# Performance work log

Hardware: AMD Instinct MI355X
Metric: run time of the kernel (lower is better)

Reference implementation:

```python
import jax, jax.numpy as jnp
import numpy as np

B, T, D_Q, D_K, D_W = 128, 4096, 16, 16, 32


def setup_inputs() -> dict:
    key0 = jax.random.key(0)
    ks = jax.random.split(key0, 8)
    return {
        "query": jax.random.normal(ks[0], (B, 1, D_Q), dtype=jnp.float32),
        "key": jax.random.normal(ks[1], (B, T, D_K), dtype=jnp.float32),
        "value": jax.random.normal(ks[2], (B, T, D_K), dtype=jnp.float32),
        "W1": jax.random.normal(ks[3], (D_W, D_Q), dtype=jnp.float32) * 0.1,
        "W2": jax.random.normal(ks[4], (D_W, D_K), dtype=jnp.float32) * 0.1,
        "bias": jax.random.uniform(ks[5], (), dtype=jnp.float32, minval=-0.1, maxval=0.1),
        "v_w": jax.random.normal(ks[6], (1, D_W), dtype=jnp.float32) * 0.1,
        "v_b": jax.random.normal(ks[7], (1,), dtype=jnp.float32) * 0.1,
    }


def reference(query, key, value, W1, W2, bias, v_w, v_b):
    # Bahdanau additive attention.
    # query: [B,1,d_q], key/value: [B,T,d_k]
    q_proj = jnp.einsum('bqd,wd->bqw', query, W1)      # [B,1,d_w]
    k_proj = jnp.einsum('btd,wd->btw', key, W2)        # [B,T,d_w]
    h = jnp.tanh(k_proj + q_proj + bias)               # [B,T,d_w]
    score = (jnp.einsum('btw,ow->bto', h, v_w) + v_b).squeeze(-1)  # [B,T]
    attn = jax.nn.softmax(score, axis=-1)              # [B,T]
    context = jnp.einsum('bt,btd->bd', attn, value)[:, None, :]    # [B,1,d_v]
    return context, attn
```

## Files before the change

### kernel.cpp

```cpp
#include <hip/hip_runtime.h>

#define NB 128
#define NT 4096
#define DKD 16
#define DW 32
#define CHUNKS 16
#define TC 256
#define BLK 256
#define BLK2 128

__device__ __forceinline__ float fast_tanh(float x) {
    float e = __expf(2.0f * x);
    return 1.0f - 2.0f * __builtin_amdgcn_rcpf(e + 1.0f);
}

__global__ __launch_bounds__(BLK, 6) void aa_score(
    const float* __restrict__ query, const float* __restrict__ key,
    const float* __restrict__ value, const float* __restrict__ W1,
    const float* __restrict__ W2, const float* __restrict__ bias,
    const float* __restrict__ v_w, const float* __restrict__ v_b,
    float* __restrict__ attn,
    float* __restrict__ ws_l,
    float* __restrict__ ws_ctx)
{
    const int b   = blockIdx.x >> 4;
    const int c   = blockIdx.x & 15;
    const int tid = threadIdx.x;

    __shared__ float s_comb[DW];
    __shared__ float s_rctx[4 * 16];
    __shared__ float s_rl[4];

    const size_t tbase = (size_t)b * NT + (size_t)c * TC + tid;
    const float4* kp = reinterpret_cast<const float4*>(key)   + tbase * 4;
    const float4* vp = reinterpret_cast<const float4*>(value) + tbase * 4;
    const float4 k0 = kp[0], k1 = kp[1], k2 = kp[2], k3 = kp[3];

    if (tid < DW) {
        const int w = tid;
        float acc = bias[0];
        const float* q  = query + b * DKD;
        const float* w1 = W1 + w * DKD;
        #pragma unroll
        for (int d = 0; d < DKD; ++d) acc = fmaf(q[d], w1[d], acc);
        s_comb[w] = acc;
    }
    __syncthreads();

    const float vb = v_b[0];
    float sc = vb;

    #pragma unroll
    for (int w = 0; w < DW; ++w) {
        const float* wr = W2 + w * DKD;
        float h = s_comb[w];
        h = fmaf(k0.x, wr[ 0], h); h = fmaf(k0.y, wr[ 1], h);
        h = fmaf(k0.z, wr[ 2], h); h = fmaf(k0.w, wr[ 3], h);
        h = fmaf(k1.x, wr[ 4], h); h = fmaf(k1.y, wr[ 5], h);
        h = fmaf(k1.z, wr[ 6], h); h = fmaf(k1.w, wr[ 7], h);
        h = fmaf(k2.x, wr[ 8], h); h = fmaf(k2.y, wr[ 9], h);
        h = fmaf(k2.z, wr[10], h); h = fmaf(k2.w, wr[11], h);
        h = fmaf(k3.x, wr[12], h); h = fmaf(k3.y, wr[13], h);
        h = fmaf(k3.z, wr[14], h); h = fmaf(k3.w, wr[15], h);
        sc = fmaf(fast_tanh(h), v_w[w], sc);
    }

    const float p = __expf(sc);
    attn[(size_t)b * NT + (size_t)c * TC + tid] = p;

    const float4 v0 = vp[0], v1 = vp[1], v2 = vp[2], v3 = vp[3];
    float ctx[16];
    ctx[ 0] = p * v0.x; ctx[ 1] = p * v0.y; ctx[ 2] = p * v0.z; ctx[ 3] = p * v0.w;
    ctx[ 4] = p * v1.x; ctx[ 5] = p * v1.y; ctx[ 6] = p * v1.z; ctx[ 7] = p * v1.w;
    ctx[ 8] = p * v2.x; ctx[ 9] = p * v2.y; ctx[10] = p * v2.z; ctx[11] = p * v2.w;
    ctx[12] = p * v3.x; ctx[13] = p * v3.y; ctx[14] = p * v3.z; ctx[15] = p * v3.w;

    float l = p;
    #pragma unroll
    for (int o = 32; o > 0; o >>= 1) l += __shfl_xor(l, o);
    #pragma unroll
    for (int d = 0; d < 16; ++d) {
        #pragma unroll
        for (int o = 32; o > 0; o >>= 1) ctx[d] += __shfl_xor(ctx[d], o);
    }
    const int wave = tid >> 6;
    const int lane = tid & 63;
    if (lane == 0) {
        s_rl[wave] = l;
        #pragma unroll
        for (int d = 0; d < 16; ++d) s_rctx[wave * 16 + d] = ctx[d];
    }
    __syncthreads();
    const int slot = b * CHUNKS + c;
    if (tid < 16)
        ws_ctx[slot * 16 + tid] =
            s_rctx[tid] + s_rctx[16 + tid] + s_rctx[32 + tid] + s_rctx[48 + tid];
    if (tid == 0)
        ws_l[slot] = s_rl[0] + s_rl[1] + s_rl[2] + s_rl[3];
}

__global__ __launch_bounds__(BLK2) void aa_finish(
    float* __restrict__ out,
    const float* __restrict__ ws_l,
    const float* __restrict__ ws_ctx)
{
    const int b   = blockIdx.x >> 3;
    const int seg = blockIdx.x & 7;
    const int tid = threadIdx.x;
    float L = 0.0f;
    #pragma unroll
    for (int i = 0; i < CHUNKS; ++i) L += ws_l[b * CHUNKS + i];
    const float inv = 1.0f / L;

    float4* ap = reinterpret_cast<float4*>(out + NB*DKD + (size_t)b * NT + (size_t)seg * 512);
    float4 p = ap[tid];
    p.x *= inv; p.y *= inv; p.z *= inv; p.w *= inv;
    ap[tid] = p;

    if (seg == 0 && tid < DKD) {
        const float* wc = ws_ctx + b * CHUNKS * 16;
        float s = 0.0f;
        #pragma unroll
        for (int i = 0; i < CHUNKS; ++i) s += wc[i * 16 + tid];
        out[b * DKD + tid] = s * inv;
    }
}

extern "C" void kernel_launch(void* const* d_in, const int* in_sizes, int n_in,
                              void* d_out, int out_size, void* d_ws, size_t ws_size,
                              hipStream_t stream) {
    const float* query = (const float*)d_in[0];
    const float* key   = (const float*)d_in[1];
    const float* value = (const float*)d_in[2];
    const float* W1    = (const float*)d_in[3];
    const float* W2    = (const float*)d_in[4];
    const float* bias  = (const float*)d_in[5];
    const float* v_w   = (const float*)d_in[6];
    const float* v_b   = (const float*)d_in[7];
    float* out = (float*)d_out;

    float* ws_l   = (float*)d_ws;
    float* ws_ctx = ws_l + NB * CHUNKS;

    aa_score<<<NB * CHUNKS, BLK, 0, stream>>>(
        query, key, value, W1, W2, bias, v_w, v_b,
        out + NB * DKD, ws_l, ws_ctx);
    aa_finish<<<NB * 8, BLK2, 0, stream>>>(out, ws_l, ws_ctx);
}
```

Measured before the change: 120.1 us.

## Fuse score and finish kernels into one block per batch row

Replaces the two-kernel scheme (chunked partial sums plus a finishing kernel) with a single kernel that gives each batch row one 1024-thread block. Each thread now processes four timesteps, and the normalisation and context reduction happen in shared memory. This removes the second launch, the workspace round-trip, and the re-read and re-write of the attention array. In exchange the grid shrinks to 128 blocks, which may leave many compute units idle for what is largely a compute-heavy tanh workload, and each thread's key and value loads become less coalesced.

```diff
diff --git a/kernel.cpp b/kernel.cpp
--- a/kernel.cpp
+++ b/kernel.cpp
@@ -4,37 +4,27 @@
 #define NT 4096
 #define DKD 16
 #define DW 32
-#define CHUNKS 16
-#define TC 256
-#define BLK 256
-#define BLK2 128
+#define BLK 1024
+#define PT 4
 
 __device__ __forceinline__ float fast_tanh(float x) {
     float e = __expf(2.0f * x);
     return 1.0f - 2.0f * __builtin_amdgcn_rcpf(e + 1.0f);
 }
 
-__global__ __launch_bounds__(BLK, 6) void aa_score(
+__global__ __launch_bounds__(BLK, 1) void aa_fused(
     const float* __restrict__ query, const float* __restrict__ key,
     const float* __restrict__ value, const float* __restrict__ W1,
     const float* __restrict__ W2, const float* __restrict__ bias,
     const float* __restrict__ v_w, const float* __restrict__ v_b,
-    float* __restrict__ attn,
-    float* __restrict__ ws_l,
-    float* __restrict__ ws_ctx)
+    float* __restrict__ out)
 {
-    const int b   = blockIdx.x >> 4;
-    const int c   = blockIdx.x & 15;
+    const int b   = blockIdx.x;
     const int tid = threadIdx.x;
 
     __shared__ float s_comb[DW];
-    __shared__ float s_rctx[4 * 16];
-    __shared__ float s_rl[4];
-
-    const size_t tbase = (size_t)b * NT + (size_t)c * TC + tid;
-    const float4* kp = reinterpret_cast<const float4*>(key)   + tbase * 4;
-    const float4* vp = reinterpret_cast<const float4*>(value) + tbase * 4;
-    const float4 k0 = kp[0], k1 = kp[1], k2 = kp[2], k3 = kp[3];
+    __shared__ float s_rl[16];
+    __shared__ float s_rctx[16 * 16];
 
     if (tid < DW) {
         const int w = tid;
@@ -48,34 +38,50 @@
     __syncthreads();
 
     const float vb = v_b[0];
-    float sc = vb;
+    const float4* kp = reinterpret_cast<const float4*>(key)   + ((size_t)b * NT + tid * PT) * 4;
+    const float4* vp = reinterpret_cast<const float4*>(value) + ((size_t)b * NT + tid * PT) * 4;
+
+    float p[PT];
+    float l = 0.0f;
+    float ctx[16];
+    #pragma unroll
+    for (int d = 0; d < 16; ++d) ctx[d] = 0.0f;
 
     #pragma unroll
-    for (int w = 0; w < DW; ++w) {
-        const float* wr = W2 + w * DKD;
-        float h = s_comb[w];
-        h = fmaf(k0.x, wr[ 0], h); h = fmaf(k0.y, wr[ 1], h);
-        h = fmaf(k0.z, wr[ 2], h); h = fmaf(k0.w, wr[ 3], h);
-        h = fmaf(k1.x, wr[ 4], h); h = fmaf(k1.y, wr[ 5], h);
-        h = fmaf(k1.z, wr[ 6], h); h = fmaf(k1.w, wr[ 7], h);
-        h = fmaf(k2.x, wr[ 8], h); h = fmaf(k2.y, wr[ 9], h);
-        h = fmaf(k2.z, wr[10], h); h = fmaf(k2.w, wr[11], h);
-        h = fmaf(k3.x, wr[12], h); h = fmaf(k3.y, wr[13], h);
-        h = fmaf(k3.z, wr[14], h); h = fmaf(k3.w, wr[15], h);
-        sc = fmaf(fast_tanh(h), v_w[w], sc);
+    for (int j = 0; j < PT; ++j) {
+        const float4 k0 = kp[4*j + 0], k1 = kp[4*j + 1];
+        const float4 k2 = kp[4*j + 2], k3 = kp[4*j + 3];
+
+        float sc = vb;
+        #pragma unroll
+        for (int w = 0; w < DW; ++w) {
+            const float* wr = W2 + w * DKD;
+            float h = s_comb[w];
+            h = fmaf(k0.x, wr[ 0], h); h = fmaf(k0.y, wr[ 1], h);
+            h = fmaf(k0.z, wr[ 2], h); h = fmaf(k0.w, wr[ 3], h);
+            h = fmaf(k1.x, wr[ 4], h); h = fmaf(k1.y, wr[ 5], h);
+            h = fmaf(k1.z, wr[ 6], h); h = fmaf(k1.w, wr[ 7], h);
+            h = fmaf(k2.x, wr[ 8], h); h = fmaf(k2.y, wr[ 9], h);
+            h = fmaf(k2.z, wr[10], h); h = fmaf(k2.w, wr[11], h);
+            h = fmaf(k3.x, wr[12], h); h = fmaf(k3.y, wr[13], h);
+            h = fmaf(k3.z, wr[14], h); h = fmaf(k3.w, wr[15], h);
+            sc = fmaf(fast_tanh(h), v_w[w], sc);
+        }
+        p[j] = __expf(sc);
+        l += p[j];
+
+        const float4 v0 = vp[4*j + 0], v1 = vp[4*j + 1];
+        const float4 v2 = vp[4*j + 2], v3 = vp[4*j + 3];
+        ctx[ 0] = fmaf(p[j], v0.x, ctx[ 0]); ctx[ 1] = fmaf(p[j], v0.y, ctx[ 1]);
+        ctx[ 2] = fmaf(p[j], v0.z, ctx[ 2]); ctx[ 3] = fmaf(p[j], v0.w, ctx[ 3]);
+        ctx[ 4] = fmaf(p[j], v1.x, ctx[ 4]); ctx[ 5] = fmaf(p[j], v1.y, ctx[ 5]);
+        ctx[ 6] = fmaf(p[j], v1.z, ctx[ 6]); ctx[ 7] = fmaf(p[j], v1.w, ctx[ 7]);
+        ctx[ 8] = fmaf(p[j], v2.x, ctx[ 8]); ctx[ 9] = fmaf(p[j], v2.y, ctx[ 9]);
+        ctx[10] = fmaf(p[j], v2.z, ctx[10]); ctx[11] = fmaf(p[j], v2.w, ctx[11]);
+        ctx[12] = fmaf(p[j], v3.x, ctx[12]); ctx[13] = fmaf(p[j], v3.y, ctx[13]);
+        ctx[14] = fmaf(p[j], v3.z, ctx[14]); ctx[15] = fmaf(p[j], v3.w, ctx[15]);
     }
 
-    const float p = __expf(sc);
-    attn[(size_t)b * NT + (size_t)c * TC + tid] = p;
-
-    const float4 v0 = vp[0], v1 = vp[1], v2 = vp[2], v3 = vp[3];
-    float ctx[16];
-    ctx[ 0] = p * v0.x; ctx[ 1] = p * v0.y; ctx[ 2] = p * v0.z; ctx[ 3] = p * v0.w;
-    ctx[ 4] = p * v1.x; ctx[ 5] = p * v1.y; ctx[ 6] = p * v1.z; ctx[ 7] = p * v1.w;
-    ctx[ 8] = p * v2.x; ctx[ 9] = p * v2.y; ctx[10] = p * v2.z; ctx[11] = p * v2.w;
-    ctx[12] = p * v3.x; ctx[13] = p * v3.y; ctx[14] = p * v3.z; ctx[15] = p * v3.w;
-
-    float l = p;
     #pragma unroll
     for (int o = 32; o > 0; o >>= 1) l += __shfl_xor(l, o);
     #pragma unroll
@@ -91,37 +97,19 @@
         for (int d = 0; d < 16; ++d) s_rctx[wave * 16 + d] = ctx[d];
     }
     __syncthreads();
-    const int slot = b * CHUNKS + c;
-    if (tid < 16)
-        ws_ctx[slot * 16 + tid] =
-            s_rctx[tid] + s_rctx[16 + tid] + s_rctx[32 + tid] + s_rctx[48 + tid];
-    if (tid == 0)
-        ws_l[slot] = s_rl[0] + s_rl[1] + s_rl[2] + s_rl[3];
-}
 
-__global__ __launch_bounds__(BLK2) void aa_finish(
-    float* __restrict__ out,
-    const float* __restrict__ ws_l,
-    const float* __restrict__ ws_ctx)
-{
-    const int b   = blockIdx.x >> 3;
-    const int seg = blockIdx.x & 7;
-    const int tid = threadIdx.x;
     float L = 0.0f;
     #pragma unroll
-    for (int i = 0; i < CHUNKS; ++i) L += ws_l[b * CHUNKS + i];
+    for (int w = 0; w < 16; ++w) L += s_rl[w];
     const float inv = 1.0f / L;
 
-    float4* ap = reinterpret_cast<float4*>(out + NB*DKD + (size_t)b * NT + (size_t)seg * 512);
-    float4 p = ap[tid];
-    p.x *= inv; p.y *= inv; p.z *= inv; p.w *= inv;
-    ap[tid] = p;
+    reinterpret_cast<float4*>(out + NB * DKD + (size_t)b * NT)[tid] =
+        make_float4(p[0] * inv, p[1] * inv, p[2] * inv, p[3] * inv);
 
-    if (seg == 0 && tid < DKD) {
-        const float* wc = ws_ctx + b * CHUNKS * 16;
+    if (tid < DKD) {
         float s = 0.0f;
         #pragma unroll
-        for (int i = 0; i < CHUNKS; ++i) s += wc[i * 16 + tid];
+        for (int w = 0; w < 16; ++w) s += s_rctx[w * 16 + tid];
         out[b * DKD + tid] = s * inv;
     }
 }
@@ -139,11 +127,6 @@
     const float* v_b   = (const float*)d_in[7];
     float* out = (float*)d_out;
 
-    float* ws_l   = (float*)d_ws;
-    float* ws_ctx = ws_l + NB * CHUNKS;
-
-    aa_score<<<NB * CHUNKS, BLK, 0, stream>>>(
-        query, key, value, W1, W2, bias, v_w, v_b,
-        out + NB * DKD, ws_l, ws_ctx);
-    aa_finish<<<NB * 8, BLK2, 0, stream>>>(out, ws_l, ws_ctx);
+    aa_fused<<<NB, BLK, 0, stream>>>(query, key, value, W1, W2, bias,
+                                     v_w, v_b, out);
 }
```

Result: slower. 139.9 us (+16.5%).
